# Optimization experiments

Hardware: AMD Instinct MI355X
Metric: run time of the kernel (lower is better)

Reference implementation:

```python
import jax, jax.numpy as jnp
import numpy as np

HIDDEN = 768; HEADS = 8; D = HIDDEN // HEADS; L = 2
N_PAPER, N_AUTHOR = 50000, 20000
E = 100000
SQRT_D = float(np.sqrt(D))


def setup_inputs() -> dict:
    key = jax.random.key(0)
    ks = jax.random.split(key, 16)
    s = 0.05
    return {
        "x_paper": jax.random.normal(ks[0], (N_PAPER, HIDDEN), jnp.float32),
        "x_author": jax.random.normal(ks[1], (N_AUTHOR, HIDDEN), jnp.float32),
        "node_lin_W": jax.random.normal(ks[2], (2, HIDDEN, HIDDEN), jnp.float32) * s,
        "node_lin_b": jnp.zeros((2, HIDDEN), jnp.float32),
        "kqva_W": jax.random.normal(ks[3], (L, 2, 4, HIDDEN, HIDDEN), jnp.float32) * s,
        "kqva_b": jnp.zeros((L, 2, 4, HIDDEN), jnp.float32),
        "skip_param": jnp.ones((L, 2), jnp.float32),
        "a_rel": jax.random.normal(ks[4], (L, 3, HEADS, D, D), jnp.float32) * s,
        "m_rel": jax.random.normal(ks[5], (L, 3, HEADS, D, D), jnp.float32) * s,
        "p_rel": jnp.ones((L, 3, HEADS), jnp.float32),
        "ei_pp_src": jax.random.randint(ks[6], (E,), 0, N_PAPER, jnp.int32),
        "ei_pp_dst": jax.random.randint(ks[7], (E,), 0, N_PAPER, jnp.int32),
        "ei_ap_src": jax.random.randint(ks[8], (E,), 0, N_AUTHOR, jnp.int32),
        "ei_ap_dst": jax.random.randint(ks[9], (E,), 0, N_PAPER, jnp.int32),
        "ei_pa_src": jax.random.randint(ks[10], (E,), 0, N_PAPER, jnp.int32),
        "ei_pa_dst": jax.random.randint(ks[11], (E,), 0, N_AUTHOR, jnp.int32),
    }


def _segment_softmax(logits, seg, num_segments):
    # logits: [E, H]; softmax over edges sharing the same destination node
    m = jax.ops.segment_max(logits, seg, num_segments=num_segments)
    e = jnp.exp(logits - m[seg])
    denom = jax.ops.segment_sum(e, seg, num_segments=num_segments)
    return e / (denom[seg] + 1e-16)


def _hgt_layer(h, lW, lb, skip, aR, mR, pR, edges, ns):
    # h: list of per-node-type features [N_t, HIDDEN]
    # lW: [2, 4, HIDDEN, HIDDEN] (k, q, v, a per node type); lb: [2, 4, HIDDEN]
    kqv = []
    for t in range(2):
        k = (h[t] @ lW[t, 0] + lb[t, 0]).reshape(-1, HEADS, D)
        q = (h[t] @ lW[t, 1] + lb[t, 1]).reshape(-1, HEADS, D)
        v = (h[t] @ lW[t, 2] + lb[t, 2]).reshape(-1, HEADS, D)
        kqv.append((k, q, v))
    aggr = [jnp.zeros((ns[t], HEADS, D), h[0].dtype) for t in range(2)]
    for e, (st, dt, src, dst) in enumerate(edges):
        k_src, _, v_src = kqv[st]
        q_dst = kqv[dt][1]
        # relation-specific key/message transforms: [E,H,D] x [H,D,D] -> [E,H,D]
        ke = jnp.einsum('ehd,hdf->ehf', k_src[src], aR[e])
        alpha = (q_dst[dst] * ke).sum(-1) * pR[e] / SQRT_D  # [E, H]
        alpha = _segment_softmax(alpha, dst, ns[dt])
        msg = jnp.einsum('ehd,hdf->ehf', v_src[src], mR[e]) * alpha[..., None]
        aggr[dt] = aggr[dt] + jax.ops.segment_sum(msg, dst, num_segments=ns[dt])
    out = []
    for t in range(2):
        o = jax.nn.gelu(aggr[t].reshape(ns[t], HIDDEN), approximate=False) @ lW[t, 3] + lb[t, 3]
        beta = jax.nn.sigmoid(skip[t])
        out.append(beta * o + (1.0 - beta) * h[t])
    return out


def reference(x_paper, x_author, node_lin_W, node_lin_b, kqva_W, kqva_b, skip_param,
              a_rel, m_rel, p_rel,
              ei_pp_src, ei_pp_dst, ei_ap_src, ei_ap_dst, ei_pa_src, ei_pa_dst):
    ns = (x_paper.shape[0], x_author.shape[0])
    h = [jax.nn.relu(x_paper @ node_lin_W[0] + node_lin_b[0]),
         jax.nn.relu(x_author @ node_lin_W[1] + node_lin_b[1])]
    # (src_type, dst_type, src_idx, dst_idx) per edge type
    edges = [(0, 0, ei_pp_src, ei_pp_dst),
             (1, 0, ei_ap_src, ei_ap_dst),
             (0, 1, ei_pa_src, ei_pa_dst)]
    for l in range(L):
        h = _hgt_layer(h, kqva_W[l], kqva_b[l], skip_param[l],
                       a_rel[l], m_rel[l], p_rel[l], edges, ns)
        h = [jax.nn.relu(t) for t in h]  # dropout = identity (eval mode)
    return (h[0], h[1])
```

## Files before the change

kernel.cpp:

```cpp
#include <hip/hip_runtime.h>
#include <cstdio>
#include <cmath>

#define HIDDEN 768
#define HEADS 8
#define DHEAD 96
#define NLAYERS 2
#define HH (HIDDEN * HIDDEN)

typedef unsigned short u16;
typedef unsigned int u32;
typedef __attribute__((ext_vector_type(8))) short bf16x8;
typedef __attribute__((ext_vector_type(4))) float f32x4;

__device__ __forceinline__ u16 f2b(float f) {
    u32 u = __float_as_uint(f);
    u32 r = (u + 0x7FFFu + ((u >> 16) & 1u)) >> 16;
    return (u16)r;
}
__device__ __forceinline__ float b2f(u16 v) { return __uint_as_float(((u32)v) << 16); }

template<int OUTF, int OUTB, int ACT>
__global__ __launch_bounds__(256, 3)
void gemm_mfma(const u16* __restrict__ A, const u16* __restrict__ Wt,
               const float* __restrict__ bias,
               float* __restrict__ Cf, u16* __restrict__ Cb,
               int M, int N, int K)
{
    __shared__ u16 As[128 * 32];
    __shared__ u16 Bs[128 * 32];
    const int tid = threadIdx.x;
    const int lane = tid & 63;
    const int wave = tid >> 6;
    const long m0 = (long)blockIdx.x * 128;
    const long n0 = (long)blockIdx.y * 128;
    const int wm = (wave & 1) * 64;
    const int wn = (wave >> 1) * 64;

    f32x4 acc[4][4];
#pragma unroll
    for (int i = 0; i < 4; i++)
#pragma unroll
        for (int j = 0; j < 4; j++) acc[i][j] = (f32x4){0.f, 0.f, 0.f, 0.f};

    const int r0 = tid >> 2, p0 = tid & 3;
    const int g0 = p0 ^ ((r0 >> 1) & 3);
    const int r1 = r0 + 64;
    const int g1 = p0 ^ ((r1 >> 1) & 3);
    const u16* ga0 = A + (m0 + r0) * (long)K + g0 * 8;
    const u16* ga1 = A + (m0 + r1) * (long)K + g1 * 8;
    const u16* gb0 = Wt + (n0 + r0) * (long)K + g0 * 8;
    const u16* gb1 = Wt + (n0 + r1) * (long)K + g1 * 8;
    u16* la0 = As + tid * 8;
    u16* la1 = As + (tid + 256) * 8;
    u16* lb0 = Bs + tid * 8;
    u16* lb1 = Bs + (tid + 256) * 8;

    for (int k0 = 0; k0 < K; k0 += 32) {
        __builtin_amdgcn_global_load_lds((const __attribute__((address_space(1))) void*)(ga0 + k0),
                                         (__attribute__((address_space(3))) void*)la0, 16, 0, 0);
        __builtin_amdgcn_global_load_lds((const __attribute__((address_space(1))) void*)(ga1 + k0),
                                         (__attribute__((address_space(3))) void*)la1, 16, 0, 0);
        __builtin_amdgcn_global_load_lds((const __attribute__((address_space(1))) void*)(gb0 + k0),
                                         (__attribute__((address_space(3))) void*)lb0, 16, 0, 0);
        __builtin_amdgcn_global_load_lds((const __attribute__((address_space(1))) void*)(gb1 + k0),
                                         (__attribute__((address_space(3))) void*)lb1, 16, 0, 0);
        __syncthreads();

        bf16x8 af[4], bfr[4];
        const int q = lane >> 4;
        const int lr = lane & 15;
#pragma unroll
        for (int i = 0; i < 4; i++) {
            int rr = wm + i * 16 + lr;
            af[i] = *(const bf16x8*)(As + rr * 32 + ((q ^ ((rr >> 1) & 3)) * 8));
            int rn = wn + i * 16 + lr;
            bfr[i] = *(const bf16x8*)(Bs + rn * 32 + ((q ^ ((rn >> 1) & 3)) * 8));
        }
#pragma unroll
        for (int i = 0; i < 4; i++)
#pragma unroll
            for (int j = 0; j < 4; j++)
                acc[i][j] = __builtin_amdgcn_mfma_f32_16x16x32_bf16(af[i], bfr[j], acc[i][j], 0, 0, 0);
        __syncthreads();
    }

    const int lc = lane & 15, lq = lane >> 4;
#pragma unroll
    for (int j = 0; j < 4; j++) {
        long col = n0 + wn + j * 16 + lc;
        float bv = bias ? bias[col] : 0.f;
#pragma unroll
        for (int i = 0; i < 4; i++) {
#pragma unroll
            for (int rg = 0; rg < 4; rg++) {
                long row = m0 + wm + i * 16 + lq * 4 + rg;
                float v = acc[i][j][rg] + bv;
                if (ACT) v = fmaxf(v, 0.f);
                if (OUTF) Cf[row * N + col] = v;
                if (OUTB) Cb[row * N + col] = f2b(v);
            }
        }
    }
}

template<int ACT>
__global__ void gemm_f32(const float* __restrict__ A, int lda, long sA,
                         const float* __restrict__ W, int ldw, long sW,
                         const float* __restrict__ bias, long sB,
                         float* __restrict__ C, int ldc, long sC,
                         int M, int N, int K)
{
    int bz = blockIdx.z;
    A += (long)bz * sA;
    W += (long)bz * sW;
    C += (long)bz * sC;
    if (bias) bias += (long)bz * sB;

    __shared__ float Ash[16][65];
    __shared__ float Wsh[16][65];

    int tid = threadIdx.x;
    int tx = tid & 15, ty = tid >> 4;
    int m0 = blockIdx.x * 64, n0 = blockIdx.y * 64;
    float acc[4][4] = {};

    for (int k0 = 0; k0 < K; k0 += 16) {
#pragma unroll
        for (int i = 0; i < 4; i++) {
            int t = tid + i * 256;
            int mm = t >> 4, kk = t & 15;
            int gm = m0 + mm;
            Ash[kk][mm] = (gm < M) ? A[(long)gm * lda + (k0 + kk)] : 0.f;
        }
#pragma unroll
        for (int i = 0; i < 4; i++) {
            int t = tid + i * 256;
            int kk = t >> 6, nn = t & 63;
            int gn = n0 + nn;
            Wsh[kk][nn] = (gn < N) ? W[(long)(k0 + kk) * ldw + gn] : 0.f;
        }
        __syncthreads();
#pragma unroll
        for (int kk = 0; kk < 16; kk++) {
            float a[4], w[4];
#pragma unroll
            for (int i = 0; i < 4; i++) a[i] = Ash[kk][ty * 4 + i];
#pragma unroll
            for (int j = 0; j < 4; j++) w[j] = Wsh[kk][tx * 4 + j];
#pragma unroll
            for (int i = 0; i < 4; i++)
#pragma unroll
                for (int j = 0; j < 4; j++) acc[i][j] = fmaf(a[i], w[j], acc[i][j]);
        }
        __syncthreads();
    }
#pragma unroll
    for (int i = 0; i < 4; i++) {
        int gm = m0 + ty * 4 + i;
        if (gm >= M) continue;
#pragma unroll
        for (int j = 0; j < 4; j++) {
            int gn = n0 + tx * 4 + j;
            if (gn >= N) continue;
            float v = acc[i][j];
            if (bias) v += bias[gn];
            if (ACT == 1) v = fmaxf(v, 0.f);
            C[(long)gm * ldc + gn] = v;
        }
    }
}

__global__ void transpose_f2b(const float* __restrict__ src, long sStride,
                              u16* __restrict__ dst, long dStride)
{
    __shared__ float t[32][33];
    int z = blockIdx.z;
    src += (long)z * sStride;
    dst += (long)z * dStride;
    int bx = blockIdx.x * 32, by = blockIdx.y * 32;
    int x = threadIdx.x, y = threadIdx.y;
#pragma unroll
    for (int i = 0; i < 32; i += 8)
        t[y + i][x] = src[(long)(by + y + i) * 768 + bx + x];
    __syncthreads();
#pragma unroll
    for (int i = 0; i < 32; i += 8)
        dst[(long)(bx + y + i) * 768 + by + x] = f2b(t[x][y + i]);
}

__global__ void bias_comb_k(const float* __restrict__ kb, const float* __restrict__ aR,
                            const float* __restrict__ mR, float* __restrict__ bc)
{
    int idx = blockIdx.x * blockDim.x + threadIdx.x;
    if (idx >= 12 * 768) return;
    int combo = idx / 768;
    int x = idx % 768;
    int h = x / 96, j = x % 96;
    int c6 = combo % 6;
    int l = c6 / 3, e = c6 % 3;
    int kind = (combo < 6) ? 0 : 2;
    int st = (e == 1) ? 1 : 0;
    const float* R = ((combo < 6) ? aR : mR) + ((long)(l * 3 + e) * 8 + h) * 9216;
    const float* kbp = kb + ((long)(l * 2 + st) * 4 + kind) * 768 + h * 96;
    float s = 0.f;
#pragma unroll 8
    for (int d = 0; d < 96; d++) s = fmaf(kbp[d], R[d * 96 + j], s);
    bc[idx] = s;
}

__global__ void conv_pad(const float* __restrict__ src, u16* __restrict__ dst,
                         long nReal, long nPad)
{
    long i = blockIdx.x * (long)blockDim.x + threadIdx.x;
    if (i >= nPad) return;
    dst[i] = (i < nReal) ? f2b(src[i]) : (u16)0;
}

__global__ void fill_f32(float* __restrict__ p, float v, long n) {
    long i = blockIdx.x * (long)blockDim.x + threadIdx.x;
    if (i < n) p[i] = v;
}

__global__ void skip_k(const float* __restrict__ o, const u16* __restrict__ hin,
                       const float* __restrict__ sp, u16* __restrict__ outb,
                       float* __restrict__ outf, long n)
{
    long i = blockIdx.x * (long)blockDim.x + threadIdx.x;
    if (i < n) {
        float beta = 1.f / (1.f + expf(-sp[0]));
        float v = beta * o[i] + (1.f - beta) * b2f(hin[i]);
        v = fmaxf(v, 0.f);
        outb[i] = f2b(v);
        if (outf) outf[i] = v;
    }
}

__device__ __forceinline__ float bdot(u32 a, u32 b, float s) {
    float al = __uint_as_float(a << 16);
    float ah = __uint_as_float(a & 0xffff0000u);
    float bl = __uint_as_float(b << 16);
    float bh = __uint_as_float(b & 0xffff0000u);
    return fmaf(ah, bh, fmaf(al, bl, s));
}

__global__ void edge_logits(const u16* __restrict__ q, const u16* __restrict__ kt,
                            const int* __restrict__ src, const int* __restrict__ dst,
                            const float* __restrict__ prel, float* __restrict__ out,
                            int ne)
{
    int idx = blockIdx.x * blockDim.x + threadIdx.x;
    if (idx >= ne * HEADS) return;
    int e = idx >> 3, h = idx & 7;
    const u16* qr = q + (long)dst[e] * HIDDEN + h * DHEAD;
    const u16* kr = kt + (long)src[e] * HIDDEN + h * DHEAD;
    float s = 0.f;
#pragma unroll
    for (int c = 0; c < 12; c++) {
        uint4 qv = *(const uint4*)(qr + c * 8);
        uint4 kv = *(const uint4*)(kr + c * 8);
        s = bdot(qv.x, kv.x, s);
        s = bdot(qv.y, kv.y, s);
        s = bdot(qv.z, kv.z, s);
        s = bdot(qv.w, kv.w, s);
    }
    out[idx] = s * prel[h] * 0.1020620726159658f;
}

__device__ __forceinline__ void atomicMaxF(float* addr, float val) {
    int* ia = (int*)addr;
    int cur = __float_as_int(*addr);
    while (__int_as_float(cur) < val) {
        int assumed = cur;
        cur = atomicCAS(ia, assumed, __float_as_int(val));
        if (cur == assumed) break;
    }
}

__global__ void seg_max_k(const float* __restrict__ lg, const int* __restrict__ dst,
                          float* __restrict__ dmax, int ne) {
    int idx = blockIdx.x * blockDim.x + threadIdx.x;
    if (idx >= ne * HEADS) return;
    int e = idx >> 3, h = idx & 7;
    atomicMaxF(&dmax[(long)dst[e] * HEADS + h], lg[idx]);
}

__global__ void seg_expsum_k(float* __restrict__ lg, const int* __restrict__ dst,
                             const float* __restrict__ dmax, float* __restrict__ denom,
                             int ne) {
    int idx = blockIdx.x * blockDim.x + threadIdx.x;
    if (idx >= ne * HEADS) return;
    int e = idx >> 3, h = idx & 7;
    float v = expf(lg[idx] - dmax[(long)dst[e] * HEADS + h]);
    lg[idx] = v;
    atomicAdd(&denom[(long)dst[e] * HEADS + h], v);
}

__global__ void hist_k(const int* __restrict__ dst, int* __restrict__ cnt, int ne) {
    int i = blockIdx.x * blockDim.x + threadIdx.x;
    if (i < ne) atomicAdd(&cnt[dst[i]], 1);
}

__global__ void excl_scan_k(const int* __restrict__ in, int* __restrict__ out, int n)
{
    __shared__ int lds[1024];
    __shared__ int carry_s;
    const int tid = threadIdx.x;
    if (tid == 0) carry_s = 0;
    __syncthreads();
    for (int base = 0; base < n; base += 8192) {
        int v[8];
        int s = 0;
        const int i0 = base + tid * 8;
#pragma unroll
        for (int j = 0; j < 8; j++) {
            v[j] = s;
            int idx = i0 + j;
            s += (idx < n) ? in[idx] : 0;
        }
        lds[tid] = s;
        __syncthreads();
        int cb = carry_s;
        for (int ofs = 1; ofs < 1024; ofs <<= 1) {
            int t = (tid >= ofs) ? lds[tid - ofs] : 0;
            __syncthreads();
            if (tid >= ofs) lds[tid] += t;
            __syncthreads();
        }
        int excl = cb + (tid ? lds[tid - 1] : 0);
#pragma unroll
        for (int j = 0; j < 8; j++) {
            int idx = i0 + j;
            if (idx < n) out[idx] = excl + v[j];
        }
        __syncthreads();
        if (tid == 0) carry_s = cb + lds[1023];
        __syncthreads();
    }
    if (tid == 0) out[n] = carry_s;
}

__global__ void scatter_perm_k(const int* __restrict__ dst, const int* __restrict__ rs,
                               int* __restrict__ cur, int* __restrict__ ep, int ne) {
    int i = blockIdx.x * blockDim.x + threadIdx.x;
    if (i < ne) {
        int d = dst[i];
        int p = rs[d] + atomicAdd(&cur[d], 1);
        ep[p] = i;
    }
}

__device__ __forceinline__ void fma4bf(uint2 pv, float a, float acc[4]) {
    acc[0] = fmaf(a, __uint_as_float(pv.x << 16), acc[0]);
    acc[1] = fmaf(a, __uint_as_float(pv.x & 0xffff0000u), acc[1]);
    acc[2] = fmaf(a, __uint_as_float(pv.y << 16), acc[2]);
    acc[3] = fmaf(a, __uint_as_float(pv.y & 0xffff0000u), acc[3]);
}

template<int NSET>
__global__ void gather_gelu_k(
    const int* __restrict__ rs0, const int* __restrict__ ep0, const int* __restrict__ src0,
    const float* __restrict__ al0, const float* __restrict__ den0, const u16* __restrict__ vt0,
    const int* __restrict__ rs1, const int* __restrict__ ep1, const int* __restrict__ src1,
    const float* __restrict__ al1, const float* __restrict__ den1, const u16* __restrict__ vt1,
    u16* __restrict__ out, int nsReal)
{
    const int node = blockIdx.x;
    const int tid = threadIdx.x;
    const int h = tid / 24;
    float acc[4] = {0.f, 0.f, 0.f, 0.f};
    if (node < nsReal) {
        {
            const int b = rs0[node], en = rs0[node + 1];
            float part[4] = {0.f, 0.f, 0.f, 0.f};
            for (int i = b; i < en; i++) {
                const int eid = ep0[i];
                const float a = al0[(long)eid * HEADS + h];
                const uint2 pv = *(const uint2*)(vt0 + (long)src0[eid] * HIDDEN + tid * 4);
                fma4bf(pv, a, part);
            }
            const float r = 1.f / (den0[(long)node * HEADS + h] + 1e-16f);
#pragma unroll
            for (int j = 0; j < 4; j++) acc[j] = part[j] * r;
        }
        if (NSET == 2) {
            const int b = rs1[node], en = rs1[node + 1];
            float part[4] = {0.f, 0.f, 0.f, 0.f};
            for (int i = b; i < en; i++) {
                const int eid = ep1[i];
                const float a = al1[(long)eid * HEADS + h];
                const uint2 pv = *(const uint2*)(vt1 + (long)src1[eid] * HIDDEN + tid * 4);
                fma4bf(pv, a, part);
            }
            const float r = 1.f / (den1[(long)node * HEADS + h] + 1e-16f);
#pragma unroll
            for (int j = 0; j < 4; j++) acc[j] = fmaf(part[j], r, acc[j]);
        }
    }
    float g[4];
#pragma unroll
    for (int j = 0; j < 4; j++)
        g[j] = 0.5f * acc[j] * (1.f + erff(acc[j] * 0.70710678118654752f));
    u32 w0 = (u32)f2b(g[0]) | ((u32)f2b(g[1]) << 16);
    u32 w1 = (u32)f2b(g[2]) | ((u32)f2b(g[3]) << 16);
    *(uint2*)(out + (long)node * HIDDEN + tid * 4) = make_uint2(w0, w1);
}

static inline void mfma_bf16out(hipStream_t s, const u16* A, const u16* Wt,
                                const float* bias, u16* Cb, int M, int act) {
    dim3 grid(M / 128, HIDDEN / 128);
    if (act)
        gemm_mfma<0, 1, 1><<<grid, 256, 0, s>>>(A, Wt, bias, nullptr, Cb, M, HIDDEN, HIDDEN);
    else
        gemm_mfma<0, 1, 0><<<grid, 256, 0, s>>>(A, Wt, bias, nullptr, Cb, M, HIDDEN, HIDDEN);
}
static inline void mfma_f32out(hipStream_t s, const u16* A, const u16* Wt,
                               const float* bias, float* Cf, int M) {
    dim3 grid(M / 128, HIDDEN / 128);
    gemm_mfma<1, 0, 0><<<grid, 256, 0, s>>>(A, Wt, bias, Cf, nullptr, M, HIDDEN, HIDDEN);
}

extern "C" void kernel_launch(void* const* d_in, const int* in_sizes, int n_in,
                              void* d_out, int out_size, void* d_ws, size_t ws_size,
                              hipStream_t stream)
{
    const float* x0  = (const float*)d_in[0];
    const float* x1  = (const float*)d_in[1];
    const float* nlW = (const float*)d_in[2];
    const float* nlb = (const float*)d_in[3];
    const float* kW  = (const float*)d_in[4];
    const float* kb  = (const float*)d_in[5];
    const float* skp = (const float*)d_in[6];
    const float* aR  = (const float*)d_in[7];
    const float* mR  = (const float*)d_in[8];
    const float* pR  = (const float*)d_in[9];
    const int* esrc[3] = {(const int*)d_in[10], (const int*)d_in[12], (const int*)d_in[14]};
    const int* edst[3] = {(const int*)d_in[11], (const int*)d_in[13], (const int*)d_in[15]};
    const int EST[3] = {0, 1, 0};
    const int EDT[3] = {0, 0, 1};
    const int EN[3]  = {in_sizes[10], in_sizes[12], in_sizes[14]};

    const int NP = in_sizes[0] / HIDDEN;
    const int NA = in_sizes[1] / HIDDEN;
    const int ns[2]    = {NP, NA};
    const int nspad[2] = {(NP + 127) & ~127, (NA + 127) & ~127};

    char* base = (char*)d_ws;
    size_t off = 0;
    auto alloc = [&](size_t bytes) -> void* {
        void* p = base + off;
        off += (bytes + 255) & ~(size_t)255;
        return p;
    };
    u16* hbf[2] = {(u16*)alloc((size_t)nspad[0] * HIDDEN * 2),
                   (u16*)alloc((size_t)nspad[1] * HIDDEN * 2)};
    u16* qbf[2] = {(u16*)alloc((size_t)nspad[0] * HIDDEN * 2),
                   (u16*)alloc((size_t)nspad[1] * HIDDEN * 2)};
    u16* ktvbase = (u16*)alloc((size_t)(2 * nspad[0] + nspad[1]) * HIDDEN * 2);
    u16* ktv[3] = {ktvbase, ktvbase + (size_t)nspad[0] * HIDDEN,
                   ktvbase + (size_t)(nspad[0] + nspad[1]) * HIDDEN};
    float* Obuf = (float*)ktvbase;
    float* alphab[3];
    for (int e = 0; e < 3; e++) alphab[e] = (float*)alloc((size_t)EN[e] * HEADS * 4);
    float* dmax = (float*)alloc((size_t)nspad[0] * HEADS * 4);
    float* denomE[3];
    for (int e = 0; e < 3; e++) denomE[e] = (float*)alloc((size_t)nspad[EDT[e]] * HEADS * 4);
    int* csr_rs[3];
    int* csr_ep[3];
    for (int e = 0; e < 3; e++) {
        csr_rs[e] = (int*)alloc((size_t)(ns[EDT[e]] + 1) * 4);
        csr_ep[e] = (int*)alloc((size_t)EN[e] * 4);
    }
    int nsMax = ns[0] > ns[1] ? ns[0] : ns[1];
    int* cursor = (int*)alloc((size_t)nsMax * 4);
    u16* Wbf     = (u16*)alloc((size_t)22 * HH * 2);
    float* Wcomb = (float*)alloc((size_t)12 * HH * 4);
    float* bcomb = (float*)alloc((size_t)12 * 768 * 4);
    if (off > ws_size)
        fprintf(stderr, "kernel_launch: ws too small: need %zu have %zu\n", off, ws_size);

    auto wslot = [&](int s) { return Wbf + (size_t)s * HH; };

    for (int e = 0; e < 3; e++) {
        int dt = EDT[e], Ne = EN[e], nd = ns[dt];
        hipMemsetAsync(cursor, 0, (size_t)nd * 4, stream);
        hist_k<<<(Ne + 255) / 256, 256, 0, stream>>>(edst[e], cursor, Ne);
        excl_scan_k<<<1, 1024, 0, stream>>>(cursor, csr_rs[e], nd);
        hipMemsetAsync(cursor, 0, (size_t)nd * 4, stream);
        scatter_perm_k<<<(Ne + 255) / 256, 256, 0, stream>>>(edst[e], csr_rs[e], cursor,
                                                             csr_ep[e], Ne);
    }

    for (int l = 0; l < NLAYERS; l++)
        for (int e = 0; e < 3; e++) {
            int st = EST[e];
            {
                const float* Ap = kW + ((size_t)(l * 2 + st) * 4 + 0) * HH;
                const float* Wp = aR + ((size_t)(l * 3 + e)) * 8 * 9216;
                float* Cp = Wcomb + (size_t)(l * 3 + e) * HH;
                dim3 g(12, 2, 8);
                gemm_f32<0><<<g, 256, 0, stream>>>(Ap, 768, 96, Wp, 96, 9216,
                                                   nullptr, 0, Cp, 768, 96, 768, 96, 96);
            }
            {
                const float* Ap = kW + ((size_t)(l * 2 + st) * 4 + 2) * HH;
                const float* Wp = mR + ((size_t)(l * 3 + e)) * 8 * 9216;
                float* Cp = Wcomb + (size_t)(6 + l * 3 + e) * HH;
                dim3 g(12, 2, 8);
                gemm_f32<0><<<g, 256, 0, stream>>>(Ap, 768, 96, Wp, 96, 9216,
                                                   nullptr, 0, Cp, 768, 96, 768, 96, 96);
            }
        }
    bias_comb_k<<<(12 * 768 + 255) / 256, 256, 0, stream>>>(kb, aR, mR, bcomb);

    {
        dim3 b(32, 8);
        dim3 g(24, 24, 2);
        transpose_f2b<<<g, b, 0, stream>>>(nlW, HH, wslot(0), HH);
        g.z = 4;
        transpose_f2b<<<g, b, 0, stream>>>(kW + (size_t)1 * HH, 4 * (long)HH, wslot(2), HH);
        transpose_f2b<<<g, b, 0, stream>>>(kW + (size_t)3 * HH, 4 * (long)HH, wslot(6), HH);
        g.z = 6;
        transpose_f2b<<<g, b, 0, stream>>>(Wcomb, HH, wslot(10), HH);
        transpose_f2b<<<g, b, 0, stream>>>(Wcomb + (size_t)6 * HH, HH, wslot(16), HH);
    }

    for (int t = 0; t < 2; t++) {
        long nPad = (long)nspad[t] * HIDDEN, nReal = (long)ns[t] * HIDDEN;
        conv_pad<<<(int)((nPad + 255) / 256), 256, 0, stream>>>(t ? x1 : x0, qbf[t], nReal, nPad);
        mfma_bf16out(stream, qbf[t], wslot(t), nlb + (size_t)t * 768, hbf[t], nspad[t], 1);
    }

    for (int l = 0; l < NLAYERS; l++) {
        for (int t = 0; t < 2; t++)
            mfma_bf16out(stream, hbf[t], wslot(2 + l * 2 + t),
                         kb + ((size_t)(l * 2 + t) * 4 + 1) * 768, qbf[t], nspad[t], 0);
        for (int e = 0; e < 3; e++) {
            int st = EST[e], dt = EDT[e], Ne = EN[e];
            mfma_bf16out(stream, hbf[st], wslot(10 + l * 3 + e),
                         bcomb + (size_t)(l * 3 + e) * 768, ktv[e], nspad[st], 0);
            int nthr = Ne * HEADS;
            edge_logits<<<(nthr + 255) / 256, 256, 0, stream>>>(
                qbf[dt], ktv[e], esrc[e], edst[e],
                pR + ((size_t)l * 3 + e) * HEADS, alphab[e], Ne);
            long nd = (long)ns[dt] * HEADS;
            fill_f32<<<(int)((nd + 255) / 256), 256, 0, stream>>>(dmax, -INFINITY, nd);
            hipMemsetAsync(denomE[e], 0, nd * sizeof(float), stream);
            seg_max_k<<<(nthr + 255) / 256, 256, 0, stream>>>(alphab[e], edst[e], dmax, Ne);
            seg_expsum_k<<<(nthr + 255) / 256, 256, 0, stream>>>(alphab[e], edst[e], dmax,
                                                                 denomE[e], Ne);
        }
        for (int e = 0; e < 3; e++) {
            int st = EST[e];
            mfma_bf16out(stream, hbf[st], wslot(16 + l * 3 + e),
                         bcomb + (size_t)(6 + l * 3 + e) * 768, ktv[e], nspad[st], 0);
        }
        gather_gelu_k<2><<<nspad[0], 192, 0, stream>>>(
            csr_rs[0], csr_ep[0], esrc[0], alphab[0], denomE[0], ktv[0],
            csr_rs[1], csr_ep[1], esrc[1], alphab[1], denomE[1], ktv[1],
            qbf[0], ns[0]);
        gather_gelu_k<1><<<nspad[1], 192, 0, stream>>>(
            csr_rs[2], csr_ep[2], esrc[2], alphab[2], denomE[2], ktv[2],
            nullptr, nullptr, nullptr, nullptr, nullptr, nullptr,
            qbf[1], ns[1]);
        for (int t = 0; t < 2; t++) {
            long nReal = (long)ns[t] * HIDDEN;
            mfma_f32out(stream, qbf[t], wslot(6 + l * 2 + t),
                        kb + ((size_t)(l * 2 + t) * 4 + 3) * 768, Obuf, nspad[t]);
            float* outf = (l == NLAYERS - 1)
                        ? ((float*)d_out + (t == 0 ? 0 : (size_t)NP * HIDDEN))
                        : nullptr;
            skip_k<<<(int)((nReal + 255) / 256), 256, 0, stream>>>(
                Obuf, hbf[t], skp + (size_t)l * 2 + t, hbf[t], outf, nReal);
        }
    }
}
```

Baseline: 3.931 ms.

## Fuse skip into output GEMM, CSR segment softmax, and transposed weight-combine output

```diff
diff --git a/kernel.cpp b/kernel.cpp
--- a/kernel.cpp
+++ b/kernel.cpp
@@ -104,17 +104,106 @@
     }
 }
 
-template<int ACT>
+template<int OUTF>
+__global__ __launch_bounds__(256, 3)
+void gemm_skip(const u16* __restrict__ A, const u16* __restrict__ Wt,
+               const float* __restrict__ bias, const u16* __restrict__ hprev,
+               const float* __restrict__ sp, u16* __restrict__ hout,
+               float* __restrict__ outf, int M, int N, int K, int nReal)
+{
+    __shared__ u16 As[128 * 32];
+    __shared__ u16 Bs[128 * 32];
+    const int tid = threadIdx.x;
+    const int lane = tid & 63;
+    const int wave = tid >> 6;
+    const long m0 = (long)blockIdx.x * 128;
+    const long n0 = (long)blockIdx.y * 128;
+    const int wm = (wave & 1) * 64;
+    const int wn = (wave >> 1) * 64;
+
+    f32x4 acc[4][4];
+#pragma unroll
+    for (int i = 0; i < 4; i++)
+#pragma unroll
+        for (int j = 0; j < 4; j++) acc[i][j] = (f32x4){0.f, 0.f, 0.f, 0.f};
+
+    const int r0 = tid >> 2, p0 = tid & 3;
+    const int g0 = p0 ^ ((r0 >> 1) & 3);
+    const int r1 = r0 + 64;
+    const int g1 = p0 ^ ((r1 >> 1) & 3);
+    const u16* ga0 = A + (m0 + r0) * (long)K + g0 * 8;
+    const u16* ga1 = A + (m0 + r1) * (long)K + g1 * 8;
+    const u16* gb0 = Wt + (n0 + r0) * (long)K + g0 * 8;
+    const u16* gb1 = Wt + (n0 + r1) * (long)K + g1 * 8;
+    u16* la0 = As + tid * 8;
+    u16* la1 = As + (tid + 256) * 8;
+    u16* lb0 = Bs + tid * 8;
+    u16* lb1 = Bs + (tid + 256) * 8;
+
+    for (int k0 = 0; k0 < K; k0 += 32) {
+        __builtin_amdgcn_global_load_lds((const __attribute__((address_space(1))) void*)(ga0 + k0),
+                                         (__attribute__((address_space(3))) void*)la0, 16, 0, 0);
+        __builtin_amdgcn_global_load_lds((const __attribute__((address_space(1))) void*)(ga1 + k0),
+                                         (__attribute__((address_space(3))) void*)la1, 16, 0, 0);
+        __builtin_amdgcn_global_load_lds((const __attribute__((address_space(1))) void*)(gb0 + k0),
+                                         (__attribute__((address_space(3))) void*)lb0, 16, 0, 0);
+        __builtin_amdgcn_global_load_lds((const __attribute__((address_space(1))) void*)(gb1 + k0),
+                                         (__attribute__((address_space(3))) void*)lb1, 16, 0, 0);
+        __syncthreads();
+
+        bf16x8 af[4], bfr[4];
+        const int q = lane >> 4;
+        const int lr = lane & 15;
+#pragma unroll
+        for (int i = 0; i < 4; i++) {
+            int rr = wm + i * 16 + lr;
+            af[i] = *(const bf16x8*)(As + rr * 32 + ((q ^ ((rr >> 1) & 3)) * 8));
+            int rn = wn + i * 16 + lr;
+            bfr[i] = *(const bf16x8*)(Bs + rn * 32 + ((q ^ ((rn >> 1) & 3)) * 8));
+        }
+#pragma unroll
+        for (int i = 0; i < 4; i++)
+#pragma unroll
+            for (int j = 0; j < 4; j++)
+                acc[i][j] = __builtin_amdgcn_mfma_f32_16x16x32_bf16(af[i], bfr[j], acc[i][j], 0, 0, 0);
+        __syncthreads();
+    }
+
+    const float beta = 1.f / (1.f + expf(-sp[0]));
+    const int lc = lane & 15, lq = lane >> 4;
+#pragma unroll
+    for (int j = 0; j < 4; j++) {
+        long col = n0 + wn + j * 16 + lc;
+        float bv = bias[col];
+#pragma unroll
+        for (int i = 0; i < 4; i++) {
+#pragma unroll
+            for (int rg = 0; rg < 4; rg++) {
+                long row = m0 + wm + i * 16 + lq * 4 + rg;
+                if (row < nReal) {
+                    float o = acc[i][j][rg] + bv;
+                    float v = beta * o + (1.f - beta) * b2f(hprev[row * N + col]);
+                    v = fmaxf(v, 0.f);
+                    hout[row * N + col] = f2b(v);
+                    if (OUTF) outf[row * N + col] = v;
+                }
+            }
+        }
+    }
+}
+
+template<int ACT, int OUTT>
 __global__ void gemm_f32(const float* __restrict__ A, int lda, long sA,
                          const float* __restrict__ W, int ldw, long sW,
                          const float* __restrict__ bias, long sB,
                          float* __restrict__ C, int ldc, long sC,
+                         u16* __restrict__ Ct,
                          int M, int N, int K)
 {
     int bz = blockIdx.z;
     A += (long)bz * sA;
     W += (long)bz * sW;
-    C += (long)bz * sC;
+    if (!OUTT) C += (long)bz * sC;
     if (bias) bias += (long)bz * sB;
 
     __shared__ float Ash[16][65];
@@ -166,7 +255,10 @@
             float v = acc[i][j];
             if (bias) v += bias[gn];
             if (ACT == 1) v = fmaxf(v, 0.f);
-            C[(long)gm * ldc + gn] = v;
+            if (OUTT)
+                Ct[(long)(bz * N + gn) * M + gm] = f2b(v);
+            else
+                C[(long)gm * ldc + gn] = v;
         }
     }
 }
@@ -217,25 +309,6 @@
     dst[i] = (i < nReal) ? f2b(src[i]) : (u16)0;
 }
 
-__global__ void fill_f32(float* __restrict__ p, float v, long n) {
-    long i = blockIdx.x * (long)blockDim.x + threadIdx.x;
-    if (i < n) p[i] = v;
-}
-
-__global__ void skip_k(const float* __restrict__ o, const u16* __restrict__ hin,
-                       const float* __restrict__ sp, u16* __restrict__ outb,
-                       float* __restrict__ outf, long n)
-{
-    long i = blockIdx.x * (long)blockDim.x + threadIdx.x;
-    if (i < n) {
-        float beta = 1.f / (1.f + expf(-sp[0]));
-        float v = beta * o[i] + (1.f - beta) * b2f(hin[i]);
-        v = fmaxf(v, 0.f);
-        outb[i] = f2b(v);
-        if (outf) outf[i] = v;
-    }
-}
-
 __device__ __forceinline__ float bdot(u32 a, u32 b, float s) {
     float al = __uint_as_float(a << 16);
     float ah = __uint_as_float(a & 0xffff0000u);
@@ -267,33 +340,34 @@
     out[idx] = s * prel[h] * 0.1020620726159658f;
 }
 
-__device__ __forceinline__ void atomicMaxF(float* addr, float val) {
-    int* ia = (int*)addr;
-    int cur = __float_as_int(*addr);
-    while (__int_as_float(cur) < val) {
-        int assumed = cur;
-        cur = atomicCAS(ia, assumed, __float_as_int(val));
-        if (cur == assumed) break;
-    }
-}
-
-__global__ void seg_max_k(const float* __restrict__ lg, const int* __restrict__ dst,
-                          float* __restrict__ dmax, int ne) {
-    int idx = blockIdx.x * blockDim.x + threadIdx.x;
-    if (idx >= ne * HEADS) return;
-    int e = idx >> 3, h = idx & 7;
-    atomicMaxF(&dmax[(long)dst[e] * HEADS + h], lg[idx]);
-}
-
-__global__ void seg_expsum_k(float* __restrict__ lg, const int* __restrict__ dst,
-                             const float* __restrict__ dmax, float* __restrict__ denom,
-                             int ne) {
-    int idx = blockIdx.x * blockDim.x + threadIdx.x;
-    if (idx >= ne * HEADS) return;
-    int e = idx >> 3, h = idx & 7;
-    float v = expf(lg[idx] - dmax[(long)dst[e] * HEADS + h]);
-    lg[idx] = v;
-    atomicAdd(&denom[(long)dst[e] * HEADS + h], v);
+__global__ void csr_softmax_k(const int* __restrict__ rs, const int* __restrict__ ep,
+                              float* __restrict__ alpha, int nnodes)
+{
+    int wid = (blockIdx.x * blockDim.x + threadIdx.x) >> 6;
+    if (wid >= nnodes) return;
+    const int lane = threadIdx.x & 63;
+    const int h = lane >> 3, slot = lane & 7;
+    const int b = rs[wid], en = rs[wid + 1];
+
+    float m = -INFINITY;
+    for (int i = b + slot; i < en; i += 8)
+        m = fmaxf(m, alpha[(long)ep[i] * HEADS + h]);
+    m = fmaxf(m, __shfl_xor(m, 1));
+    m = fmaxf(m, __shfl_xor(m, 2));
+    m = fmaxf(m, __shfl_xor(m, 4));
+
+    float s = 0.f;
+    for (int i = b + slot; i < en; i += 8)
+        s += expf(alpha[(long)ep[i] * HEADS + h] - m);
+    s += __shfl_xor(s, 1);
+    s += __shfl_xor(s, 2);
+    s += __shfl_xor(s, 4);
+    const float inv = 1.f / (s + 1e-16f);
+
+    for (int i = b + slot; i < en; i += 8) {
+        long idx = (long)ep[i] * HEADS + h;
+        alpha[idx] = expf(alpha[idx] - m) * inv;
+    }
 }
 
 __global__ void hist_k(const int* __restrict__ dst, int* __restrict__ cnt, int ne) {
@@ -360,9 +434,9 @@
 template<int NSET>
 __global__ void gather_gelu_k(
     const int* __restrict__ rs0, const int* __restrict__ ep0, const int* __restrict__ src0,
-    const float* __restrict__ al0, const float* __restrict__ den0, const u16* __restrict__ vt0,
+    const float* __restrict__ al0, const u16* __restrict__ vt0,
     const int* __restrict__ rs1, const int* __restrict__ ep1, const int* __restrict__ src1,
-    const float* __restrict__ al1, const float* __restrict__ den1, const u16* __restrict__ vt1,
+    const float* __restrict__ al1, const u16* __restrict__ vt1,
     u16* __restrict__ out, int nsReal)
 {
     const int node = blockIdx.x;
@@ -372,29 +446,21 @@
     if (node < nsReal) {
         {
             const int b = rs0[node], en = rs0[node + 1];
-            float part[4] = {0.f, 0.f, 0.f, 0.f};
             for (int i = b; i < en; i++) {
                 const int eid = ep0[i];
                 const float a = al0[(long)eid * HEADS + h];
                 const uint2 pv = *(const uint2*)(vt0 + (long)src0[eid] * HIDDEN + tid * 4);
-                fma4bf(pv, a, part);
+                fma4bf(pv, a, acc);
             }
-            const float r = 1.f / (den0[(long)node * HEADS + h] + 1e-16f);
-#pragma unroll
-            for (int j = 0; j < 4; j++) acc[j] = part[j] * r;
         }
         if (NSET == 2) {
             const int b = rs1[node], en = rs1[node + 1];
-            float part[4] = {0.f, 0.f, 0.f, 0.f};
             for (int i = b; i < en; i++) {
                 const int eid = ep1[i];
                 const float a = al1[(long)eid * HEADS + h];
                 const uint2 pv = *(const uint2*)(vt1 + (long)src1[eid] * HIDDEN + tid * 4);
-                fma4bf(pv, a, part);
+                fma4bf(pv, a, acc);
             }
-            const float r = 1.f / (den1[(long)node * HEADS + h] + 1e-16f);
-#pragma unroll
-            for (int j = 0; j < 4; j++) acc[j] = fmaf(part[j], r, acc[j]);
         }
     }
     float g[4];
@@ -413,11 +479,6 @@
         gemm_mfma<0, 1, 1><<<grid, 256, 0, s>>>(A, Wt, bias, nullptr, Cb, M, HIDDEN, HIDDEN);
     else
         gemm_mfma<0, 1, 0><<<grid, 256, 0, s>>>(A, Wt, bias, nullptr, Cb, M, HIDDEN, HIDDEN);
-}
-static inline void mfma_f32out(hipStream_t s, const u16* A, const u16* Wt,
-                               const float* bias, float* Cf, int M) {
-    dim3 grid(M / 128, HIDDEN / 128);
-    gemm_mfma<1, 0, 0><<<grid, 256, 0, s>>>(A, Wt, bias, Cf, nullptr, M, HIDDEN, HIDDEN);
 }
 
 extern "C" void kernel_launch(void* const* d_in, const int* in_sizes, int n_in,
@@ -459,12 +520,8 @@
     u16* ktvbase = (u16*)alloc((size_t)(2 * nspad[0] + nspad[1]) * HIDDEN * 2);
     u16* ktv[3] = {ktvbase, ktvbase + (size_t)nspad[0] * HIDDEN,
                    ktvbase + (size_t)(nspad[0] + nspad[1]) * HIDDEN};
-    float* Obuf = (float*)ktvbase;
     float* alphab[3];
     for (int e = 0; e < 3; e++) alphab[e] = (float*)alloc((size_t)EN[e] * HEADS * 4);
-    float* dmax = (float*)alloc((size_t)nspad[0] * HEADS * 4);
-    float* denomE[3];
-    for (int e = 0; e < 3; e++) denomE[e] = (float*)alloc((size_t)nspad[EDT[e]] * HEADS * 4);
     int* csr_rs[3];
     int* csr_ep[3];
     for (int e = 0; e < 3; e++) {
@@ -474,7 +531,6 @@
     int nsMax = ns[0] > ns[1] ? ns[0] : ns[1];
     int* cursor = (int*)alloc((size_t)nsMax * 4);
     u16* Wbf     = (u16*)alloc((size_t)22 * HH * 2);
-    float* Wcomb = (float*)alloc((size_t)12 * HH * 4);
     float* bcomb = (float*)alloc((size_t)12 * 768 * 4);
     if (off > ws_size)
         fprintf(stderr, "kernel_launch: ws too small: need %zu have %zu\n", off, ws_size);
@@ -497,18 +553,18 @@
             {
                 const float* Ap = kW + ((size_t)(l * 2 + st) * 4 + 0) * HH;
                 const float* Wp = aR + ((size_t)(l * 3 + e)) * 8 * 9216;
-                float* Cp = Wcomb + (size_t)(l * 3 + e) * HH;
                 dim3 g(12, 2, 8);
-                gemm_f32<0><<<g, 256, 0, stream>>>(Ap, 768, 96, Wp, 96, 9216,
-                                                   nullptr, 0, Cp, 768, 96, 768, 96, 96);
+                gemm_f32<0, 1><<<g, 256, 0, stream>>>(Ap, 768, 96, Wp, 96, 9216,
+                                                      nullptr, 0, nullptr, 0, 0,
+                                                      wslot(10 + l * 3 + e), 768, 96, 96);
             }
             {
                 const float* Ap = kW + ((size_t)(l * 2 + st) * 4 + 2) * HH;
                 const float* Wp = mR + ((size_t)(l * 3 + e)) * 8 * 9216;
-                float* Cp = Wcomb + (size_t)(6 + l * 3 + e) * HH;
                 dim3 g(12, 2, 8);
-                gemm_f32<0><<<g, 256, 0, stream>>>(Ap, 768, 96, Wp, 96, 9216,
-                                                   nullptr, 0, Cp, 768, 96, 768, 96, 96);
+                gemm_f32<0, 1><<<g, 256, 0, stream>>>(Ap, 768, 96, Wp, 96, 9216,
+                                                      nullptr, 0, nullptr, 0, 0,
+                                                      wslot(16 + l * 3 + e), 768, 96, 96);
             }
         }
     bias_comb_k<<<(12 * 768 + 255) / 256, 256, 0, stream>>>(kb, aR, mR, bcomb);
@@ -520,9 +576,6 @@
         g.z = 4;
         transpose_f2b<<<g, b, 0, stream>>>(kW + (size_t)1 * HH, 4 * (long)HH, wslot(2), HH);
         transpose_f2b<<<g, b, 0, stream>>>(kW + (size_t)3 * HH, 4 * (long)HH, wslot(6), HH);
-        g.z = 6;
-        transpose_f2b<<<g, b, 0, stream>>>(Wcomb, HH, wslot(10), HH);
-        transpose_f2b<<<g, b, 0, stream>>>(Wcomb + (size_t)6 * HH, HH, wslot(16), HH);
     }
 
     for (int t = 0; t < 2; t++) {
@@ -543,12 +596,8 @@
             edge_logits<<<(nthr + 255) / 256, 256, 0, stream>>>(
                 qbf[dt], ktv[e], esrc[e], edst[e],
                 pR + ((size_t)l * 3 + e) * HEADS, alphab[e], Ne);
-            long nd = (long)ns[dt] * HEADS;
-            fill_f32<<<(int)((nd + 255) / 256), 256, 0, stream>>>(dmax, -INFINITY, nd);
-            hipMemsetAsync(denomE[e], 0, nd * sizeof(float), stream);
-            seg_max_k<<<(nthr + 255) / 256, 256, 0, stream>>>(alphab[e], edst[e], dmax, Ne);
-            seg_expsum_k<<<(nthr + 255) / 256, 256, 0, stream>>>(alphab[e], edst[e], dmax,
-                                                                 denomE[e], Ne);
+            csr_softmax_k<<<(ns[dt] + 3) / 4, 256, 0, stream>>>(
+                csr_rs[e], csr_ep[e], alphab[e], ns[dt]);
         }
         for (int e = 0; e < 3; e++) {
             int st = EST[e];
@@ -556,22 +605,27 @@
                          bcomb + (size_t)(6 + l * 3 + e) * 768, ktv[e], nspad[st], 0);
         }
         gather_gelu_k<2><<<nspad[0], 192, 0, stream>>>(
-            csr_rs[0], csr_ep[0], esrc[0], alphab[0], denomE[0], ktv[0],
-            csr_rs[1], csr_ep[1], esrc[1], alphab[1], denomE[1], ktv[1],
+            csr_rs[0], csr_ep[0], esrc[0], alphab[0], ktv[0],
+            csr_rs[1], csr_ep[1], esrc[1], alphab[1], ktv[1],
             qbf[0], ns[0]);
         gather_gelu_k<1><<<nspad[1], 192, 0, stream>>>(
-            csr_rs[2], csr_ep[2], esrc[2], alphab[2], denomE[2], ktv[2],
-            nullptr, nullptr, nullptr, nullptr, nullptr, nullptr,
+            csr_rs[2], csr_ep[2], esrc[2], alphab[2], ktv[2],
+            nullptr, nullptr, nullptr, nullptr, nullptr,
             qbf[1], ns[1]);
         for (int t = 0; t < 2; t++) {
-            long nReal = (long)ns[t] * HIDDEN;
-            mfma_f32out(stream, qbf[t], wslot(6 + l * 2 + t),
-                        kb + ((size_t)(l * 2 + t) * 4 + 3) * 768, Obuf, nspad[t]);
-            float* outf = (l == NLAYERS - 1)
-                        ? ((float*)d_out + (t == 0 ? 0 : (size_t)NP * HIDDEN))
-                        : nullptr;
-            skip_k<<<(int)((nReal + 255) / 256), 256, 0, stream>>>(
-                Obuf, hbf[t], skp + (size_t)l * 2 + t, hbf[t], outf, nReal);
-        }
-    }
-}
+            dim3 grid(nspad[t] / 128, HIDDEN / 128);
+            const float* bias = kb + ((size_t)(l * 2 + t) * 4 + 3) * 768;
+            const float* sp = skp + (size_t)l * 2 + t;
+            if (l == NLAYERS - 1) {
+                float* outf = (float*)d_out + (t == 0 ? 0 : (size_t)NP * HIDDEN);
+                gemm_skip<1><<<grid, 256, 0, stream>>>(qbf[t], wslot(6 + l * 2 + t), bias,
+                                                       hbf[t], sp, hbf[t], outf,
+                                                       nspad[t], HIDDEN, HIDDEN, ns[t]);
+            } else {
+                gemm_skip<0><<<grid, 256, 0, stream>>>(qbf[t], wslot(6 + l * 2 + t), bias,
+                                                       hbf[t], sp, hbf[t], nullptr,
+                                                       nspad[t], HIDDEN, HIDDEN, ns[t]);
+            }
+        }
+    }
+}
```

Result: no change. 3.899 ms (-0.8%).
